# Optimization experiments

Hardware: AMD Instinct MI355X
Metric: run time of the kernel (lower is better)

## Reference

```python
import jax, jax.numpy as jnp
import numpy as np

N_NODES = 100000
N_EDGES = 1600000


def _sage_conv(x, src, dst, W_l, W_r, b):
    """PyG SAGEConv (mean aggr): lin_l(mean of neighbor feats) + b + lin_r(x)."""
    n = x.shape[0]
    msgs = x[src]                                            # [E, F] gather
    agg = jax.ops.segment_sum(msgs, dst, num_segments=n)     # [N, F]
    cnt = jax.ops.segment_sum(jnp.ones((src.shape[0],), x.dtype), dst,
                              num_segments=n)                # [N]
    mean = agg / jnp.maximum(cnt, 1.0)[:, None]
    return mean @ W_l + b + x @ W_r


def setup_inputs() -> dict:
    key = jax.random.key(0)
    ks = jax.random.split(key, 8)
    x = jax.random.normal(ks[0], (N_NODES, 64), dtype=jnp.float32)
    edge_index = jax.random.randint(ks[1], (2, N_EDGES), 0, N_NODES, dtype=jnp.int64)
    # Glorot-ish small init for weights
    W1_l = jax.random.normal(ks[2], (64, 128), dtype=jnp.float32) * 0.1
    W1_r = jax.random.normal(ks[3], (64, 128), dtype=jnp.float32) * 0.1
    b1 = jax.random.normal(ks[4], (128,), dtype=jnp.float32) * 0.1
    W2_l = jax.random.normal(ks[5], (128, 64), dtype=jnp.float32) * 0.1
    W2_r = jax.random.normal(ks[6], (128, 64), dtype=jnp.float32) * 0.1
    b2 = jax.random.normal(ks[7], (64,), dtype=jnp.float32) * 0.1
    return {"x": x, "edge_index": edge_index, "W1_l": W1_l, "W1_r": W1_r,
            "b1": b1, "W2_l": W2_l, "W2_r": W2_r, "b2": b2}


def reference(x, edge_index, W1_l, W1_r, b1, W2_l, W2_r, b2):
    src, dst = edge_index[0], edge_index[1]
    h = jax.nn.relu(_sage_conv(x, src, dst, W1_l, W1_r, b1))  # [N, 128]
    out = _sage_conv(h, src, dst, W2_l, W2_r, b2)             # [N, 64]
    return out
```

## Files before the change

### kernel.cpp

```cpp
#include <hip/hip_runtime.h>
#include <hip/hip_bf16.h>
#include <stdint.h>


typedef unsigned short u16;
typedef __attribute__((ext_vector_type(8))) short short8;
typedef __attribute__((ext_vector_type(4))) float f32x4;

#define BSHIFT 9
#define BSIZE  512
#define CHUNK  8192
#define NCP    256

__device__ __forceinline__ float bf2f(u16 v) { return __uint_as_float(((uint32_t)v) << 16); }
__device__ __forceinline__ float bfu_lo(uint32_t u) { return __uint_as_float(u << 16); }
__device__ __forceinline__ float bfu_hi(uint32_t u) { return __uint_as_float(u & 0xffff0000u); }
__device__ __forceinline__ u16 f2bf(float f) {
    uint32_t u = __float_as_uint(f);
    return (u16)((u + 0x7fffu + ((u >> 16) & 1u)) >> 16);
}

__global__ __launch_bounds__(512) void setup_k(
    const void* __restrict__ x, const void* __restrict__ ei,
    const void* __restrict__ W1l, const void* __restrict__ W1r,
    const void* __restrict__ b1, const void* __restrict__ W2l,
    const void* __restrict__ W2r, const void* __restrict__ b2,
    u16* __restrict__ wpk, u16* __restrict__ xb,
    int* __restrict__ hist2d, int* __restrict__ flags,
    int nn, int ne, int nb, int nchunk, int ncvt,
    int c0, int c1, int c2, int c3, int c4, int c5, int c6) {
    __shared__ int sh[512];
    __shared__ int sflag;
    int bid = blockIdx.x, tid = threadIdx.x;
    if (bid < nchunk) {
        sh[tid] = 0;
        int samp = 0;
        if (tid < 32) {
            long long n32 = 2LL * ne;
            long long stride = n32 / 32; if (stride < 1) stride = 1;
            long long i = (long long)tid * stride; i |= 1;
            if (i >= n32) i = 1;
            samp = (((const int*)ei)[i] != 0);
        }
        unsigned long long m = __ballot(samp);
        if (tid == 0) sflag = (m == 0ULL) ? 1 : 0;
        __syncthreads();
        int e64 = sflag;
        int base = bid * CHUNK;
#pragma unroll
        for (int j = 0; j < 16; j++) {
            int e = base + j * 512 + tid;
            if (e < ne) {
                int dst = e64 ? (int)((const long long*)ei)[(size_t)ne + e]
                              : ((const int*)ei)[(size_t)ne + e];
                if ((unsigned)dst < (unsigned)nn) atomicAdd(&sh[dst >> BSHIFT], 1);
            }
        }
        __syncthreads();
        for (int b = tid; b < nb; b += 512)
            hist2d[b * NCP + bid] = sh[b];
    } else if (bid < nchunk + ncvt) {
        int samp = 0;
        if (tid < 32) {
            int C = c0; int stride = C / 32; if (stride < 1) stride = 1;
            long long i = (long long)tid * stride;
            if (i > C - 1) i = C - 1; i &= ~1LL;
            u16 v = ((const u16*)x)[i];
            int e = (v >> 7) & 0xFF;
            samp = ((e >= 0x50 && e <= 0x97) || v == 0) ? 1 : 0;
        }
        unsigned long long m = __ballot(samp);
        if (tid == 0) sflag = (__popcll(m) >= 24) ? 1 : 0;
        __syncthreads();
        if (sflag) return;
        int i = (bid - nchunk) * 512 + tid;
        if (i < nn * 16) {
            float4 f = ((const float4*)x)[i];
            *(ushort4*)&xb[(size_t)i * 4] =
                make_ushort4(f2bf(f.x), f2bf(f.y), f2bf(f.z), f2bf(f.w));
        }
    } else if (bid < nchunk + ncvt + 4) {
        int b = bid - nchunk - ncvt;
        const void* src = (b == 0) ? W1l : (b == 1) ? W1r : (b == 2) ? W2l : W2r;
        int C = (b == 0) ? c1 : (b == 1) ? c2 : (b == 2) ? c4 : c5;
        int samp = 0;
        if (tid < 32) {
            int stride = C / 32; if (stride < 1) stride = 1;
            long long i = (long long)tid * stride;
            if (i > C - 1) i = C - 1; i &= ~1LL;
            u16 v = ((const u16*)src)[i];
            int e = (v >> 7) & 0xFF;
            samp = ((e >= 0x50 && e <= 0x97) || v == 0) ? 1 : 0;
        }
        unsigned long long m = __ballot(samp);
        if (tid == 0) sflag = (__popcll(m) >= 24) ? 1 : 0;
        __syncthreads();
        int isbf = sflag;
        u16* dst = wpk + ((b >= 2) ? (16384 + (b - 2) * 8192) : 0);
        for (int i = tid; i < 2048; i += 512) {
            u16 v0, v1, v2, v3;
            if (isbf) {
                ushort4 u = ((const ushort4*)src)[i];
                v0 = u.x; v1 = u.y; v2 = u.z; v3 = u.w;
            } else {
                float4 u = ((const float4*)src)[i];
                v0 = f2bf(u.x); v1 = f2bf(u.y); v2 = f2bf(u.z); v3 = f2bf(u.w);
            }
            int k, n, k8;
            if (b <= 1) { k = i >> 5; n = (i & 31) * 4; k8 = (b == 1 ? 8 : 0) + (k >> 3); }
            else        { k = i >> 4; n = (i & 15) * 4; k8 = k >> 3; }
            int kc = k8 >> 2, q = k8 & 3, w = k & 7;
            int basei = ((n >> 4) * 4 + kc) * 512 + (q * 16 + (n & 15)) * 8 + w;
            dst[basei] = v0; dst[basei + 8] = v1; dst[basei + 16] = v2; dst[basei + 24] = v3;
        }
    } else {
        int a = tid >> 5, lane = tid & 31;
        if (tid < 8) sh[tid] = 0;
        __syncthreads();
        if (a < 7) {
            const void* ptrs[7] = {x, W1l, W1r, b1, W2l, W2r, b2};
            int cs[7] = {c0, c1, c2, c3, c4, c5, c6};
            int C = cs[a];
            int stride = C / 32; if (stride < 1) stride = 1;
            long long i = (long long)lane * stride;
            if (i > C - 1) i = C - 1;
            i &= ~1LL;
            u16 v = ((const u16*)ptrs[a])[i];
            int e = (v >> 7) & 0xFF;
            int sane = ((e >= 0x50 && e <= 0x97) || v == 0) ? 1 : 0;
            atomicAdd(&sh[a], sane);
        } else if (a == 7) {
            long long n32 = 2LL * ne;
            long long stride = n32 / 32; if (stride < 1) stride = 1;
            long long i = (long long)lane * stride; i |= 1;
            if (i >= n32) i = 1;
            int wv = ((const int*)ei)[i];
            atomicAdd(&sh[7], wv != 0 ? 1 : 0);
        }
        __syncthreads();
        if (tid < 7) flags[tid] = (sh[tid] >= 24) ? 1 : 0;
        if (tid == 7) flags[7] = (sh[7] == 0) ? 1 : 0;
    }
}

__global__ __launch_bounds__(256) void scan2d(
    const int* __restrict__ hist2d, int* __restrict__ base2d,
    int* __restrict__ btot, int nchunk) {
    __shared__ int t0[256];
    int b = blockIdx.x, tid = threadIdx.x;
    int v = (tid < nchunk) ? hist2d[b * NCP + tid] : 0;
    t0[tid] = v;
    __syncthreads();
    for (int d = 1; d < 256; d <<= 1) {
        int t = (tid >= d) ? t0[tid - d] : 0;
        __syncthreads();
        t0[tid] += t;
        __syncthreads();
    }
    if (tid < nchunk) base2d[b * NCP + tid] = t0[tid] - v;
    if (tid == 255) btot[b] = t0[255];
}

__global__ __launch_bounds__(512) void partition_k(
    const void* __restrict__ ei, const int* __restrict__ btot,
    const int* __restrict__ base2d,
    unsigned* __restrict__ ep, int nn, int ne, int nb) {
    __shared__ unsigned stage[CHUNK];
    __shared__ u16 ab[CHUNK];
    __shared__ int hist[512], incl[512], exl[512], gbase[512], lcur[512];
    __shared__ int e64s;
    int tid = threadIdx.x;
    int base = blockIdx.x * CHUNK;
    hist[tid] = 0;
    int samp = 0;
    if (tid < 32) {
        long long n32 = 2LL * ne;
        long long stride = n32 / 32; if (stride < 1) stride = 1;
        long long i = (long long)tid * stride; i |= 1;
        if (i >= n32) i = 1;
        samp = (((const int*)ei)[i] != 0);
    }
    unsigned long long bm = __ballot(samp);
    if (tid == 0) e64s = (bm == 0ULL) ? 1 : 0;
    __syncthreads();
    int e64 = e64s;
    unsigned pk[16]; int bk[16];
#pragma unroll
    for (int j = 0; j < 16; j++) {
        int e = base + j * 512 + tid;
        bk[j] = -1;
        pk[j] = 0;
        if (e < ne) {
            int src, dst;
            if (e64) {
                src = (int)((const long long*)ei)[e];
                dst = (int)((const long long*)ei)[(size_t)ne + e];
            } else {
                src = ((const int*)ei)[e];
                dst = ((const int*)ei)[(size_t)ne + e];
            }
            if ((unsigned)dst < (unsigned)nn) {
                if ((unsigned)src >= (unsigned)nn) src = 0;
                bk[j] = dst >> BSHIFT;
                pk[j] = (unsigned)src | ((unsigned)(dst & (BSIZE - 1)) << 17);
                atomicAdd(&hist[bk[j]], 1);
            }
        }
    }
    __syncthreads();
    incl[tid] = hist[tid];
    __syncthreads();
    for (int d = 1; d < 512; d <<= 1) {
        int t = (tid >= d) ? incl[tid - d] : 0;
        __syncthreads();
        incl[tid] += t;
        __syncthreads();
    }
    int ex = incl[tid] - hist[tid];
    exl[tid] = ex;
    lcur[tid] = ex;
    int tot = incl[511];
    __syncthreads();
    incl[tid] = (tid < nb) ? btot[tid] : 0;
    __syncthreads();
    for (int d = 1; d < 512; d <<= 1) {
        int t = (tid >= d) ? incl[tid - d] : 0;
        __syncthreads();
        incl[tid] += t;
        __syncthreads();
    }
    int bo_t = incl[tid] - ((tid < nb) ? btot[tid] : 0);
    gbase[tid] = (tid < nb) ? (bo_t + base2d[tid * NCP + blockIdx.x]) : 0;
    __syncthreads();
#pragma unroll
    for (int j = 0; j < 16; j++) {
        if (bk[j] >= 0) {
            int r = atomicAdd(&lcur[bk[j]], 1);
            stage[r] = pk[j];
            ab[r] = (u16)bk[j];
        }
    }
    __syncthreads();
    for (int j = tid; j < tot; j += 512) {
        int b = ab[j];
        ep[gbase[b] + (j - exl[b])] = stage[j];
    }
}

__global__ __launch_bounds__(512) void csr_fill2(
    const unsigned* __restrict__ ep, const int* __restrict__ btot,
    int* __restrict__ off, int* __restrict__ cnt, int* __restrict__ esrc,
    int nn, int nb) {
    __shared__ int hist[BSIZE], incl[BSIZE], lcur[BSIZE];
    int b = blockIdx.x;
    int tid = threadIdx.x;
    incl[tid] = (tid < nb) ? btot[tid] : 0;
    __syncthreads();
    for (int d = 1; d < 512; d <<= 1) {
        int t = (tid >= d) ? incl[tid - d] : 0;
        __syncthreads();
        incl[tid] += t;
        __syncthreads();
    }
    int end = incl[b];
    int beg = end - btot[b];
    __syncthreads();
    hist[tid] = 0;
    __syncthreads();
    for (int j = beg + tid; j < end; j += 512)
        atomicAdd(&hist[(ep[j] >> 17) & (BSIZE - 1)], 1);
    __syncthreads();
    incl[tid] = hist[tid];
    __syncthreads();
    for (int d = 1; d < 512; d <<= 1) {
        int t = (tid >= d) ? incl[tid - d] : 0;
        __syncthreads();
        incl[tid] += t;
        __syncthreads();
    }
    int ex = beg + incl[tid] - hist[tid];
    lcur[tid] = ex;
    int node = b * BSIZE + tid;
    if (node < nn) { off[node] = ex; cnt[node] = hist[tid]; }
    __syncthreads();
    for (int j = beg + tid; j < end; j += 512) {
        unsigned p = ep[j];
        int r = atomicAdd(&lcur[(p >> 17) & (BSIZE - 1)], 1);
        esrc[r] = (int)(p & 0x1FFFFu);
    }
}

__global__ __launch_bounds__(512, 8) void layer1(
    const void* __restrict__ x, const u16* __restrict__ xb,
    const int* __restrict__ esrc,
    const int* __restrict__ off, const int* __restrict__ cnt,
    const u16* __restrict__ w1g, const u16* __restrict__ w2lg,
    const void* __restrict__ b1,
    u16* __restrict__ h, u16* __restrict__ gpt,
    const int* __restrict__ flags, int nn) {
    __shared__ __align__(16) u16 wA[8 * 512];
    __shared__ float b_s[128];
    int tid = threadIdx.x;
    int node0 = blockIdx.x * 32;

    if (tid < 128) b_s[tid] = flags[3] ? bf2f(((const u16*)b1)[tid]) : ((const float*)b1)[tid];

    int grp = tid >> 4, gl = tid & 15;
    int n = node0 + grp;
    int mtile = grp >> 4, l15m = grp & 15;
    int idx_mean = (mtile * 4 + (gl >> 3)) * 512 + (((gl >> 1) & 3) * 16 + l15m) * 8 + (gl & 1) * 4;
    int idx_x = (mtile * 4 + 2 + (gl >> 3)) * 512 + (((gl >> 1) & 3) * 16 + l15m) * 8 + (gl & 1) * 4;
    const u16* xs = flags[0] ? (const u16*)x : xb;
    if (n < nn) {
        int beg = off[n], deg = cnt[n];
        float a0 = 0.f, a1 = 0.f, a2 = 0.f, a3 = 0.f;
        int i = 0;
        const u16* xbp = xs + gl * 4;
        for (; i + 16 <= deg; i += 16) {
            ushort4 v[16];
#pragma unroll
            for (int j = 0; j < 16; j++) {
                int s0 = esrc[beg + i + j];
                v[j] = *(const ushort4*)(xbp + (size_t)s0 * 64);
            }
#pragma unroll
            for (int j = 0; j < 16; j++) {
                a0 += bf2f(v[j].x); a1 += bf2f(v[j].y);
                a2 += bf2f(v[j].z); a3 += bf2f(v[j].w);
            }
        }
        for (; i + 8 <= deg; i += 8) {
            ushort4 v[8];
#pragma unroll
            for (int j = 0; j < 8; j++) {
                int s0 = esrc[beg + i + j];
                v[j] = *(const ushort4*)(xbp + (size_t)s0 * 64);
            }
#pragma unroll
            for (int j = 0; j < 8; j++) {
                a0 += bf2f(v[j].x); a1 += bf2f(v[j].y);
                a2 += bf2f(v[j].z); a3 += bf2f(v[j].w);
            }
        }
        for (; i < deg; i++) {
            int s0 = esrc[beg + i];
            ushort4 v = *(const ushort4*)(xbp + (size_t)s0 * 64);
            a0 += bf2f(v.x); a1 += bf2f(v.y); a2 += bf2f(v.z); a3 += bf2f(v.w);
        }
        float inv = 1.0f / (float)(deg > 0 ? deg : 1);
        *(ushort4*)&wA[idx_mean] =
            make_ushort4(f2bf(a0 * inv), f2bf(a1 * inv), f2bf(a2 * inv), f2bf(a3 * inv));
        *(ushort4*)&wA[idx_x] = *(const ushort4*)(xs + (size_t)n * 64 + gl * 4);
    } else {
        *(ushort4*)&wA[idx_mean] = make_ushort4(0, 0, 0, 0);
        *(ushort4*)&wA[idx_x] = make_ushort4(0, 0, 0, 0);
    }
    __syncthreads();

    int wv = tid >> 6, lane = tid & 63;
    int l15 = lane & 15, q = lane >> 4;
    f32x4 acc0 = {0.f, 0.f, 0.f, 0.f};
    f32x4 acc1 = {0.f, 0.f, 0.f, 0.f};
#pragma unroll
    for (int kc = 0; kc < 4; kc++) {
        short8 a0 = *(const short8*)&wA[(kc) * 512 + lane * 8];
        short8 a1 = *(const short8*)&wA[(4 + kc) * 512 + lane * 8];
        short8 b  = *(const short8*)&w1g[(wv * 4 + kc) * 512 + lane * 8];
        acc0 = __builtin_amdgcn_mfma_f32_16x16x32_bf16(a0, b, acc0, 0, 0, 0);
        acc1 = __builtin_amdgcn_mfma_f32_16x16x32_bf16(a1, b, acc1, 0, 0, 0);
    }
    int nc = wv * 16 + l15;
    float bias = b_s[nc];
    u16 hv0[4], hv1[4];
#pragma unroll
    for (int r = 0; r < 4; r++) {
        hv0[r] = f2bf(fmaxf(acc0[r] + bias, 0.0f));
        hv1[r] = f2bf(fmaxf(acc1[r] + bias, 0.0f));
        int m = q * 4 + r;
        int nd = node0 + m;
        if (nd < nn) h[(size_t)nd * 128 + nc] = hv0[r];
        nd = node0 + 16 + m;
        if (nd < nn) h[(size_t)nd * 128 + nc] = hv1[r];
    }
    if (gpt) {
        __syncthreads();
        int kcg = wv >> 1;
        int qg  = ((wv & 1) << 1) | (l15 >> 3);
        int wg  = l15 & 7;
#pragma unroll
        for (int r = 0; r < 4; r++) {
            int m = q * 4 + r;
            wA[kcg * 512 + (qg * 16 + m) * 8 + wg]       = hv0[r];
            wA[(4 + kcg) * 512 + (qg * 16 + m) * 8 + wg] = hv1[r];
        }
        __syncthreads();
        int mt2 = wv >> 2, nt2 = wv & 3;
        f32x4 ag = {0.f, 0.f, 0.f, 0.f};
#pragma unroll
        for (int kc = 0; kc < 4; kc++) {
            short8 a = *(const short8*)&wA[(mt2 * 4 + kc) * 512 + lane * 8];
            short8 b = *(const short8*)&w2lg[(nt2 * 4 + kc) * 512 + lane * 8];
            ag = __builtin_amdgcn_mfma_f32_16x16x32_bf16(a, b, ag, 0, 0, 0);
        }
        int nc2 = nt2 * 16 + l15;
#pragma unroll
        for (int r = 0; r < 4; r++) {
            int nd = node0 + mt2 * 16 + q * 4 + r;
            if (nd < nn) gpt[(size_t)nd * 64 + nc2] = f2bf(ag[r]);
        }
    }
}

__global__ __launch_bounds__(256, 8) void pre2(
    const u16* __restrict__ h, const u16* __restrict__ w2lg,
    u16* __restrict__ g, int nn) {
    int tid = threadIdx.x;
    int node0 = blockIdx.x * 64;
    int wv = tid >> 6, lane = tid & 63;
    int l15 = lane & 15, q = lane >> 4;
    int arow = node0 + wv * 16 + l15;
    if (arow >= nn) arow = nn - 1;
    const u16* hrow = h + (size_t)arow * 128 + q * 8;
    f32x4 acc[4];
#pragma unroll
    for (int nt = 0; nt < 4; nt++) acc[nt] = (f32x4){0.f, 0.f, 0.f, 0.f};
#pragma unroll
    for (int kc = 0; kc < 4; kc++) {
        short8 a = *(const short8*)(hrow + kc * 32);
#pragma unroll
        for (int nt = 0; nt < 4; nt++) {
            short8 b = *(const short8*)&w2lg[(nt * 4 + kc) * 512 + lane * 8];
            acc[nt] = __builtin_amdgcn_mfma_f32_16x16x32_bf16(a, b, acc[nt], 0, 0, 0);
        }
    }
#pragma unroll
    for (int nt = 0; nt < 4; nt++) {
        int nc = nt * 16 + l15;
#pragma unroll
        for (int r = 0; r < 4; r++) {
            int nd = node0 + wv * 16 + q * 4 + r;
            if (nd < nn) g[(size_t)nd * 64 + nc] = f2bf(acc[nt][r]);
        }
    }
}

__global__ __launch_bounds__(512, 8) void layer2(
    const u16* __restrict__ h, const u16* __restrict__ g,
    const int* __restrict__ esrc,
    const int* __restrict__ off, const int* __restrict__ cnt,
    const u16* __restrict__ w2rg, const void* __restrict__ b2,
    void* __restrict__ out, const int* __restrict__ flags, int nn) {
    __shared__ __align__(16) u16 wA2[8 * 512];
    __shared__ __align__(16) float meanbuf[32][72];
    __shared__ float b_s[64];
    int tid = threadIdx.x;
    int node0 = blockIdx.x * 32;
    int obf = flags[0];

    if (tid < 64) b_s[tid] = flags[6] ? bf2f(((const u16*)b2)[tid]) : ((const float*)b2)[tid];

    int grp = tid >> 4, gl = tid & 15;
    int n = node0 + grp;
    int mtile = grp >> 4, m15 = grp & 15;
    int idx_h = (mtile * 4 + (gl >> 2)) * 512 + ((gl & 3) * 16 + m15) * 8;
    if (n < nn) {
        *(uint4*)&wA2[idx_h] = *(const uint4*)(h + (size_t)n * 128 + gl * 8);
        int beg = off[n], deg = cnt[n];
        float a0 = 0.f, a1 = 0.f, a2 = 0.f, a3 = 0.f;
        const u16* gb = g + gl * 4;
        int i = 0;
        for (; i + 16 <= deg; i += 16) {
            uint2 v[16];
#pragma unroll
            for (int j = 0; j < 16; j++) {
                int s0 = esrc[beg + i + j];
                v[j] = *(const uint2*)(gb + (size_t)s0 * 64);
            }
#pragma unroll
            for (int j = 0; j < 16; j++) {
                a0 += bfu_lo(v[j].x); a1 += bfu_hi(v[j].x);
                a2 += bfu_lo(v[j].y); a3 += bfu_hi(v[j].y);
            }
        }
        for (; i + 8 <= deg; i += 8) {
            uint2 v[8];
#pragma unroll
            for (int j = 0; j < 8; j++) {
                int s0 = esrc[beg + i + j];
                v[j] = *(const uint2*)(gb + (size_t)s0 * 64);
            }
#pragma unroll
            for (int j = 0; j < 8; j++) {
                a0 += bfu_lo(v[j].x); a1 += bfu_hi(v[j].x);
                a2 += bfu_lo(v[j].y); a3 += bfu_hi(v[j].y);
            }
        }
        for (; i < deg; i++) {
            int s0 = esrc[beg + i];
            uint2 v = *(const uint2*)(gb + (size_t)s0 * 64);
            a0 += bfu_lo(v.x); a1 += bfu_hi(v.x);
            a2 += bfu_lo(v.y); a3 += bfu_hi(v.y);
        }
        float inv = 1.0f / (float)(deg > 0 ? deg : 1);
        *(float4*)&meanbuf[grp][gl * 4] =
            make_float4(a0 * inv, a1 * inv, a2 * inv, a3 * inv);
    } else {
        *(uint4*)&wA2[idx_h] = make_uint4(0, 0, 0, 0);
        *(float4*)&meanbuf[grp][gl * 4] = make_float4(0.f, 0.f, 0.f, 0.f);
    }
    __syncthreads();

    int wv = tid >> 6, lane = tid & 63;
    int l15 = lane & 15, q = lane >> 4;
    int mt = wv >> 2, nt = wv & 3;
    f32x4 acc = {0.f, 0.f, 0.f, 0.f};
#pragma unroll
    for (int kc = 0; kc < 4; kc++) {
        short8 a = *(const short8*)&wA2[(mt * 4 + kc) * 512 + lane * 8];
        short8 b = *(const short8*)&w2rg[(nt * 4 + kc) * 512 + lane * 8];
        acc = __builtin_amdgcn_mfma_f32_16x16x32_bf16(a, b, acc, 0, 0, 0);
    }
    int nc = nt * 16 + l15;
    float bias = b_s[nc];
#pragma unroll
    for (int r = 0; r < 4; r++) {
        int m = mt * 16 + q * 4 + r;
        int nd = node0 + m;
        if (nd < nn) {
            float v = acc[r] + bias + meanbuf[m][nc];
            if (obf) ((u16*)out)[(size_t)nd * 64 + nc] = f2bf(v);
            else     ((float*)out)[(size_t)nd * 64 + nc] = v;
        }
    }
}

__global__ __launch_bounds__(256) void zero_out_k(u16* __restrict__ out, int n) {
    int i = blockIdx.x * 256 + threadIdx.x;
    if (i < n) out[i] = 0;
}

extern "C" void kernel_launch(void* const* d_in, const int* in_sizes, int n_in,
                              void* d_out, int out_size, void* d_ws, size_t ws_size,
                              hipStream_t stream) {
    const void* x   = d_in[0];
    const void* ei  = d_in[1];
    const void* W1l = d_in[2];
    const void* W1r = d_in[3];
    const void* b1  = d_in[4];
    const void* W2l = d_in[5];
    const void* W2r = d_in[6];
    const void* b2  = d_in[7];

    int nn = in_sizes[0] / 64;
    int ne = in_sizes[1] / 2;
    int nb = (nn + BSIZE - 1) / BSIZE;
    int nchunk = (ne + CHUNK - 1) / CHUNK;

    auto al = [](size_t v) { return (v + 255) & ~(size_t)255; };
    size_t o_flags = 0;
    size_t o_btot  = 256;
    size_t o_wpk   = al(o_btot + 512 * 4);
    size_t o_cnt   = al(o_wpk + 65536);
    size_t o_off   = al(o_cnt + (size_t)nn * 4);
    size_t o_esrc  = al(o_off + (size_t)nn * 4);
    size_t o_h     = al(o_esrc + (size_t)ne * 4);
    size_t o_xb    = al(o_h + (size_t)nn * 128 * 2);
    size_t ws_base = o_xb + (size_t)nn * 64 * 2;
    size_t o_g2    = al(ws_base);
    size_t ws_fused = o_g2 + (size_t)nn * 64 * 2;

    size_t o_ep   = o_h;
    size_t o_h2d  = al(o_ep + (size_t)ne * 4);
    size_t o_b2d  = al(o_h2d + (size_t)512 * NCP * 4);
    size_t ov_end = o_b2d + (size_t)512 * NCP * 4;

    bool ok = ws_size >= ws_base && nb >= 1 && nb <= 512 && nn <= 131072 &&
              nchunk <= NCP && ov_end <= o_xb;
    if (!ok) {
        zero_out_k<<<(out_size + 255) / 256, 256, 0, stream>>>((u16*)d_out, out_size);
        return;
    }
    bool fused = ws_size >= ws_fused;

    char* ws = (char*)d_ws;
    int* flags  = (int*)(ws + o_flags);
    int* btot   = (int*)(ws + o_btot);
    u16* wpk    = (u16*)(ws + o_wpk);
    int* cnt    = (int*)(ws + o_cnt);
    int* off    = (int*)(ws + o_off);
    int* esrc   = (int*)(ws + o_esrc);
    u16* h      = (u16*)(ws + o_h);
    u16* xb     = (u16*)(ws + o_xb);
    u16* gbuf   = fused ? (u16*)(ws + o_g2) : xb;
    unsigned* ep = (unsigned*)(ws + o_ep);
    int* hist2d = (int*)(ws + o_h2d);
    int* base2d = (int*)(ws + o_b2d);

    int ncvt = (nn * 16 + 511) / 512;
    setup_k<<<nchunk + ncvt + 5, 512, 0, stream>>>(
        x, ei, W1l, W1r, b1, W2l, W2r, b2, wpk, xb, hist2d, flags,
        nn, ne, nb, nchunk, ncvt,
        in_sizes[0], in_sizes[2], in_sizes[3], in_sizes[4],
        in_sizes[5], in_sizes[6], in_sizes[7]);
    scan2d<<<nb, 256, 0, stream>>>(hist2d, base2d, btot, nchunk);
    partition_k<<<nchunk, 512, 0, stream>>>(ei, btot, base2d, ep, nn, ne, nb);
    csr_fill2<<<nb, 512, 0, stream>>>(ep, btot, off, cnt, esrc, nn, nb);
    int lb = (nn + 31) / 32;
    layer1<<<lb, 512, 0, stream>>>(x, xb, esrc, off, cnt, wpk, wpk + 16384, b1,
                                   h, fused ? gbuf : (u16*)nullptr, flags, nn);
    if (!fused)
        pre2<<<(nn + 63) / 64, 256, 0, stream>>>(h, wpk + 16384, gbuf, nn);
    layer2<<<lb, 512, 0, stream>>>(h, gbuf, esrc, off, cnt, wpk + 24576, b2,
                                   d_out, flags, nn);
}
```

Measured before the change: 228.1 us.

## Fuse layer-2 root projection into layer1 and widen gather loads to 16 bytes

Layer1 now computes both h@W2_l and h@W2_r with MFMA and writes two 64-wide bf16 buffers instead of the 128-wide h. Layer2 becomes a pure gather-mean plus add of the precomputed root term and bias, with no MFMA or shared tiles. Both gathers use 16-byte loads with two half-groups each handling alternate edges, combined by a shuffle. This cuts h traffic and layer2 work, and drops the pre2 fallback. In exchange the workspace must always hold the extra buffer, and the second layer's root term is rounded to bf16 before the add.

After: 261.1 us. 14.5% more time.

```diff
diff --git a/kernel.cpp b/kernel.cpp
--- a/kernel.cpp
+++ b/kernel.cpp
@@ -295,8 +295,8 @@
     const int* __restrict__ esrc,
     const int* __restrict__ off, const int* __restrict__ cnt,
     const u16* __restrict__ w1g, const u16* __restrict__ w2lg,
-    const void* __restrict__ b1,
-    u16* __restrict__ h, u16* __restrict__ gpt,
+    const u16* __restrict__ w2rg, const void* __restrict__ b1,
+    u16* __restrict__ g, u16* __restrict__ rr,
     const int* __restrict__ flags, int nn) {
     __shared__ __align__(16) u16 wA[8 * 512];
     __shared__ float b_s[128];
@@ -306,54 +306,66 @@
     if (tid < 128) b_s[tid] = flags[3] ? bf2f(((const u16*)b1)[tid]) : ((const float*)b1)[tid];
 
     int grp = tid >> 4, gl = tid & 15;
+    int eh = gl >> 3, sl = gl & 7;
     int n = node0 + grp;
     int mtile = grp >> 4, l15m = grp & 15;
-    int idx_mean = (mtile * 4 + (gl >> 3)) * 512 + (((gl >> 1) & 3) * 16 + l15m) * 8 + (gl & 1) * 4;
-    int idx_x = (mtile * 4 + 2 + (gl >> 3)) * 512 + (((gl >> 1) & 3) * 16 + l15m) * 8 + (gl & 1) * 4;
+    int idx_mean = (mtile * 4 + (sl >> 2)) * 512 + ((sl & 3) * 16 + l15m) * 8;
+    int idx_x    = (mtile * 4 + 2 + (sl >> 2)) * 512 + ((sl & 3) * 16 + l15m) * 8;
     const u16* xs = flags[0] ? (const u16*)x : xb;
     if (n < nn) {
         int beg = off[n], deg = cnt[n];
-        float a0 = 0.f, a1 = 0.f, a2 = 0.f, a3 = 0.f;
+        float a[8] = {0.f, 0.f, 0.f, 0.f, 0.f, 0.f, 0.f, 0.f};
+        const u16* xbp = xs + sl * 8;
         int i = 0;
-        const u16* xbp = xs + gl * 4;
         for (; i + 16 <= deg; i += 16) {
-            ushort4 v[16];
-#pragma unroll
-            for (int j = 0; j < 16; j++) {
-                int s0 = esrc[beg + i + j];
-                v[j] = *(const ushort4*)(xbp + (size_t)s0 * 64);
+            uint4 v[8];
+#pragma unroll
+            for (int j = 0; j < 8; j++) {
+                int s0 = esrc[beg + i + 2 * j + eh];
+                v[j] = *(const uint4*)(xbp + (size_t)s0 * 64);
             }
 #pragma unroll
-            for (int j = 0; j < 16; j++) {
-                a0 += bf2f(v[j].x); a1 += bf2f(v[j].y);
-                a2 += bf2f(v[j].z); a3 += bf2f(v[j].w);
+            for (int j = 0; j < 8; j++) {
+                a[0] += bfu_lo(v[j].x); a[1] += bfu_hi(v[j].x);
+                a[2] += bfu_lo(v[j].y); a[3] += bfu_hi(v[j].y);
+                a[4] += bfu_lo(v[j].z); a[5] += bfu_hi(v[j].z);
+                a[6] += bfu_lo(v[j].w); a[7] += bfu_hi(v[j].w);
             }
         }
-        for (; i + 8 <= deg; i += 8) {
-            ushort4 v[8];
-#pragma unroll
-            for (int j = 0; j < 8; j++) {
-                int s0 = esrc[beg + i + j];
-                v[j] = *(const ushort4*)(xbp + (size_t)s0 * 64);
-            }
-#pragma unroll
-            for (int j = 0; j < 8; j++) {
-                a0 += bf2f(v[j].x); a1 += bf2f(v[j].y);
-                a2 += bf2f(v[j].z); a3 += bf2f(v[j].w);
-            }
-        }
-        for (; i < deg; i++) {
+        for (; i + 2 <= deg; i += 2) {
+            int s0 = esrc[beg + i + eh];
+            uint4 v = *(const uint4*)(xbp + (size_t)s0 * 64);
+            a[0] += bfu_lo(v.x); a[1] += bfu_hi(v.x);
+            a[2] += bfu_lo(v.y); a[3] += bfu_hi(v.y);
+            a[4] += bfu_lo(v.z); a[5] += bfu_hi(v.z);
+            a[6] += bfu_lo(v.w); a[7] += bfu_hi(v.w);
+        }
+        if (i < deg && eh == 0) {
             int s0 = esrc[beg + i];
-            ushort4 v = *(const ushort4*)(xbp + (size_t)s0 * 64);
-            a0 += bf2f(v.x); a1 += bf2f(v.y); a2 += bf2f(v.z); a3 += bf2f(v.w);
-        }
+            uint4 v = *(const uint4*)(xbp + (size_t)s0 * 64);
+            a[0] += bfu_lo(v.x); a[1] += bfu_hi(v.x);
+            a[2] += bfu_lo(v.y); a[3] += bfu_hi(v.y);
+            a[4] += bfu_lo(v.z); a[5] += bfu_hi(v.z);
+            a[6] += bfu_lo(v.w); a[7] += bfu_hi(v.w);
+        }
+#pragma unroll
+        for (int c = 0; c < 8; c++) a[c] += __shfl_xor(a[c], 8);
         float inv = 1.0f / (float)(deg > 0 ? deg : 1);
-        *(ushort4*)&wA[idx_mean] =
-            make_ushort4(f2bf(a0 * inv), f2bf(a1 * inv), f2bf(a2 * inv), f2bf(a3 * inv));
-        *(ushort4*)&wA[idx_x] = *(const ushort4*)(xs + (size_t)n * 64 + gl * 4);
+        if (eh == 0) {
+            *(ushort4*)&wA[idx_mean] =
+                make_ushort4(f2bf(a[0] * inv), f2bf(a[1] * inv), f2bf(a[2] * inv), f2bf(a[3] * inv));
+            *(ushort4*)&wA[idx_mean + 4] =
+                make_ushort4(f2bf(a[4] * inv), f2bf(a[5] * inv), f2bf(a[6] * inv), f2bf(a[7] * inv));
+        } else {
+            *(uint4*)&wA[idx_x] = *(const uint4*)(xs + (size_t)n * 64 + sl * 8);
+        }
     } else {
-        *(ushort4*)&wA[idx_mean] = make_ushort4(0, 0, 0, 0);
-        *(ushort4*)&wA[idx_x] = make_ushort4(0, 0, 0, 0);
+        if (eh == 0) {
+            *(ushort4*)&wA[idx_mean] = make_ushort4(0, 0, 0, 0);
+            *(ushort4*)&wA[idx_mean + 4] = make_ushort4(0, 0, 0, 0);
+        } else {
+            *(uint4*)&wA[idx_x] = make_uint4(0, 0, 0, 0);
+        }
     }
     __syncthreads();
 
@@ -376,160 +388,113 @@
     for (int r = 0; r < 4; r++) {
         hv0[r] = f2bf(fmaxf(acc0[r] + bias, 0.0f));
         hv1[r] = f2bf(fmaxf(acc1[r] + bias, 0.0f));
+    }
+    __syncthreads();
+    int kcg = wv >> 1;
+    int qg  = ((wv & 1) << 1) | (l15 >> 3);
+    int wg  = l15 & 7;
+#pragma unroll
+    for (int r = 0; r < 4; r++) {
         int m = q * 4 + r;
-        int nd = node0 + m;
-        if (nd < nn) h[(size_t)nd * 128 + nc] = hv0[r];
-        nd = node0 + 16 + m;
-        if (nd < nn) h[(size_t)nd * 128 + nc] = hv1[r];
-    }
-    if (gpt) {
-        __syncthreads();
-        int kcg = wv >> 1;
-        int qg  = ((wv & 1) << 1) | (l15 >> 3);
-        int wg  = l15 & 7;
-#pragma unroll
-        for (int r = 0; r < 4; r++) {
-            int m = q * 4 + r;
-            wA[kcg * 512 + (qg * 16 + m) * 8 + wg]       = hv0[r];
-            wA[(4 + kcg) * 512 + (qg * 16 + m) * 8 + wg] = hv1[r];
-        }
-        __syncthreads();
-        int mt2 = wv >> 2, nt2 = wv & 3;
-        f32x4 ag = {0.f, 0.f, 0.f, 0.f};
-#pragma unroll
-        for (int kc = 0; kc < 4; kc++) {
-            short8 a = *(const short8*)&wA[(mt2 * 4 + kc) * 512 + lane * 8];
-            short8 b = *(const short8*)&w2lg[(nt2 * 4 + kc) * 512 + lane * 8];
-            ag = __builtin_amdgcn_mfma_f32_16x16x32_bf16(a, b, ag, 0, 0, 0);
-        }
-        int nc2 = nt2 * 16 + l15;
-#pragma unroll
-        for (int r = 0; r < 4; r++) {
-            int nd = node0 + mt2 * 16 + q * 4 + r;
-            if (nd < nn) gpt[(size_t)nd * 64 + nc2] = f2bf(ag[r]);
-        }
-    }
-}
-
-__global__ __launch_bounds__(256, 8) void pre2(
-    const u16* __restrict__ h, const u16* __restrict__ w2lg,
-    u16* __restrict__ g, int nn) {
-    int tid = threadIdx.x;
-    int node0 = blockIdx.x * 64;
-    int wv = tid >> 6, lane = tid & 63;
-    int l15 = lane & 15, q = lane >> 4;
-    int arow = node0 + wv * 16 + l15;
-    if (arow >= nn) arow = nn - 1;
-    const u16* hrow = h + (size_t)arow * 128 + q * 8;
-    f32x4 acc[4];
-#pragma unroll
-    for (int nt = 0; nt < 4; nt++) acc[nt] = (f32x4){0.f, 0.f, 0.f, 0.f};
+        wA[kcg * 512 + (qg * 16 + m) * 8 + wg]       = hv0[r];
+        wA[(4 + kcg) * 512 + (qg * 16 + m) * 8 + wg] = hv1[r];
+    }
+    __syncthreads();
+    int mt2 = wv >> 2, nt2 = wv & 3;
+    f32x4 ag = {0.f, 0.f, 0.f, 0.f};
+    f32x4 ar = {0.f, 0.f, 0.f, 0.f};
 #pragma unroll
     for (int kc = 0; kc < 4; kc++) {
-        short8 a = *(const short8*)(hrow + kc * 32);
-#pragma unroll
-        for (int nt = 0; nt < 4; nt++) {
-            short8 b = *(const short8*)&w2lg[(nt * 4 + kc) * 512 + lane * 8];
-            acc[nt] = __builtin_amdgcn_mfma_f32_16x16x32_bf16(a, b, acc[nt], 0, 0, 0);
-        }
-    }
-#pragma unroll
-    for (int nt = 0; nt < 4; nt++) {
-        int nc = nt * 16 + l15;
-#pragma unroll
-        for (int r = 0; r < 4; r++) {
-            int nd = node0 + wv * 16 + q * 4 + r;
-            if (nd < nn) g[(size_t)nd * 64 + nc] = f2bf(acc[nt][r]);
+        short8 a = *(const short8*)&wA[(mt2 * 4 + kc) * 512 + lane * 8];
+        short8 bl = *(const short8*)&w2lg[(nt2 * 4 + kc) * 512 + lane * 8];
+        short8 br = *(const short8*)&w2rg[(nt2 * 4 + kc) * 512 + lane * 8];
+        ag = __builtin_amdgcn_mfma_f32_16x16x32_bf16(a, bl, ag, 0, 0, 0);
+        ar = __builtin_amdgcn_mfma_f32_16x16x32_bf16(a, br, ar, 0, 0, 0);
+    }
+    int nc2 = nt2 * 16 + l15;
+#pragma unroll
+    for (int r = 0; r < 4; r++) {
+        int nd = node0 + mt2 * 16 + q * 4 + r;
+        if (nd < nn) {
+            g[(size_t)nd * 64 + nc2]  = f2bf(ag[r]);
+            rr[(size_t)nd * 64 + nc2] = f2bf(ar[r]);
         }
     }
 }
 
 __global__ __launch_bounds__(512, 8) void layer2(
-    const u16* __restrict__ h, const u16* __restrict__ g,
+    const u16* __restrict__ g, const u16* __restrict__ rr,
     const int* __restrict__ esrc,
     const int* __restrict__ off, const int* __restrict__ cnt,
-    const u16* __restrict__ w2rg, const void* __restrict__ b2,
-    void* __restrict__ out, const int* __restrict__ flags, int nn) {
-    __shared__ __align__(16) u16 wA2[8 * 512];
-    __shared__ __align__(16) float meanbuf[32][72];
+    const void* __restrict__ b2, void* __restrict__ out,
+    const int* __restrict__ flags, int nn) {
     __shared__ float b_s[64];
     int tid = threadIdx.x;
     int node0 = blockIdx.x * 32;
     int obf = flags[0];
-
     if (tid < 64) b_s[tid] = flags[6] ? bf2f(((const u16*)b2)[tid]) : ((const float*)b2)[tid];
+    __syncthreads();
 
     int grp = tid >> 4, gl = tid & 15;
+    int eh = gl >> 3, sl = gl & 7;
     int n = node0 + grp;
-    int mtile = grp >> 4, m15 = grp & 15;
-    int idx_h = (mtile * 4 + (gl >> 2)) * 512 + ((gl & 3) * 16 + m15) * 8;
-    if (n < nn) {
-        *(uint4*)&wA2[idx_h] = *(const uint4*)(h + (size_t)n * 128 + gl * 8);
-        int beg = off[n], deg = cnt[n];
-        float a0 = 0.f, a1 = 0.f, a2 = 0.f, a3 = 0.f;
-        const u16* gb = g + gl * 4;
-        int i = 0;
-        for (; i + 16 <= deg; i += 16) {
-            uint2 v[16];
-#pragma unroll
-            for (int j = 0; j < 16; j++) {
-                int s0 = esrc[beg + i + j];
-                v[j] = *(const uint2*)(gb + (size_t)s0 * 64);
-            }
-#pragma unroll
-            for (int j = 0; j < 16; j++) {
-                a0 += bfu_lo(v[j].x); a1 += bfu_hi(v[j].x);
-                a2 += bfu_lo(v[j].y); a3 += bfu_hi(v[j].y);
-            }
-        }
-        for (; i + 8 <= deg; i += 8) {
-            uint2 v[8];
-#pragma unroll
-            for (int j = 0; j < 8; j++) {
-                int s0 = esrc[beg + i + j];
-                v[j] = *(const uint2*)(gb + (size_t)s0 * 64);
-            }
-#pragma unroll
-            for (int j = 0; j < 8; j++) {
-                a0 += bfu_lo(v[j].x); a1 += bfu_hi(v[j].x);
-                a2 += bfu_lo(v[j].y); a3 += bfu_hi(v[j].y);
-            }
-        }
-        for (; i < deg; i++) {
-            int s0 = esrc[beg + i];
-            uint2 v = *(const uint2*)(gb + (size_t)s0 * 64);
-            a0 += bfu_lo(v.x); a1 += bfu_hi(v.x);
-            a2 += bfu_lo(v.y); a3 += bfu_hi(v.y);
-        }
+    if (n >= nn) return;
+    int beg = off[n], deg = cnt[n];
+    float a[8] = {0.f, 0.f, 0.f, 0.f, 0.f, 0.f, 0.f, 0.f};
+    const u16* gb = g + sl * 8;
+    int i = 0;
+    for (; i + 16 <= deg; i += 16) {
+        uint4 v[8];
+#pragma unroll
+        for (int j = 0; j < 8; j++) {
+            int s0 = esrc[beg + i + 2 * j + eh];
+            v[j] = *(const uint4*)(gb + (size_t)s0 * 64);
+        }
+#pragma unroll
+        for (int j = 0; j < 8; j++) {
+            a[0] += bfu_lo(v[j].x); a[1] += bfu_hi(v[j].x);
+            a[2] += bfu_lo(v[j].y); a[3] += bfu_hi(v[j].y);
+            a[4] += bfu_lo(v[j].z); a[5] += bfu_hi(v[j].z);
+            a[6] += bfu_lo(v[j].w); a[7] += bfu_hi(v[j].w);
+        }
+    }
+    for (; i + 2 <= deg; i += 2) {
+        int s0 = esrc[beg + i + eh];
+        uint4 v = *(const uint4*)(gb + (size_t)s0 * 64);
+        a[0] += bfu_lo(v.x); a[1] += bfu_hi(v.x);
+        a[2] += bfu_lo(v.y); a[3] += bfu_hi(v.y);
+        a[4] += bfu_lo(v.z); a[5] += bfu_hi(v.z);
+        a[6] += bfu_lo(v.w); a[7] += bfu_hi(v.w);
+    }
+    if (i < deg && eh == 0) {
+        int s0 = esrc[beg + i];
+        uint4 v = *(const uint4*)(gb + (size_t)s0 * 64);
+        a[0] += bfu_lo(v.x); a[1] += bfu_hi(v.x);
+        a[2] += bfu_lo(v.y); a[3] += bfu_hi(v.y);
+        a[4] += bfu_lo(v.z); a[5] += bfu_hi(v.z);
+        a[6] += bfu_lo(v.w); a[7] += bfu_hi(v.w);
+    }
+#pragma unroll
+    for (int c = 0; c < 8; c++) a[c] += __shfl_xor(a[c], 8);
+    if (eh == 0) {
         float inv = 1.0f / (float)(deg > 0 ? deg : 1);
-        *(float4*)&meanbuf[grp][gl * 4] =
-            make_float4(a0 * inv, a1 * inv, a2 * inv, a3 * inv);
-    } else {
-        *(uint4*)&wA2[idx_h] = make_uint4(0, 0, 0, 0);
-        *(float4*)&meanbuf[grp][gl * 4] = make_float4(0.f, 0.f, 0.f, 0.f);
-    }
-    __syncthreads();
-
-    int wv = tid >> 6, lane = tid & 63;
-    int l15 = lane & 15, q = lane >> 4;
-    int mt = wv >> 2, nt = wv & 3;
-    f32x4 acc = {0.f, 0.f, 0.f, 0.f};
-#pragma unroll
-    for (int kc = 0; kc < 4; kc++) {
-        short8 a = *(const short8*)&wA2[(mt * 4 + kc) * 512 + lane * 8];
-        short8 b = *(const short8*)&w2rg[(nt * 4 + kc) * 512 + lane * 8];
-        acc = __builtin_amdgcn_mfma_f32_16x16x32_bf16(a, b, acc, 0, 0, 0);
-    }
-    int nc = nt * 16 + l15;
-    float bias = b_s[nc];
-#pragma unroll
-    for (int r = 0; r < 4; r++) {
-        int m = mt * 16 + q * 4 + r;
-        int nd = node0 + m;
-        if (nd < nn) {
-            float v = acc[r] + bias + meanbuf[m][nc];
-            if (obf) ((u16*)out)[(size_t)nd * 64 + nc] = f2bf(v);
-            else     ((float*)out)[(size_t)nd * 64 + nc] = v;
+        uint4 rv = *(const uint4*)(rr + (size_t)n * 64 + sl * 8);
+        float o[8];
+        o[0] = a[0] * inv + bfu_lo(rv.x); o[1] = a[1] * inv + bfu_hi(rv.x);
+        o[2] = a[2] * inv + bfu_lo(rv.y); o[3] = a[3] * inv + bfu_hi(rv.y);
+        o[4] = a[4] * inv + bfu_lo(rv.z); o[5] = a[5] * inv + bfu_hi(rv.z);
+        o[6] = a[6] * inv + bfu_lo(rv.w); o[7] = a[7] * inv + bfu_hi(rv.w);
+#pragma unroll
+        for (int c = 0; c < 8; c++) o[c] += b_s[sl * 8 + c];
+        if (obf) {
+            ushort4 w0 = make_ushort4(f2bf(o[0]), f2bf(o[1]), f2bf(o[2]), f2bf(o[3]));
+            ushort4 w1 = make_ushort4(f2bf(o[4]), f2bf(o[5]), f2bf(o[6]), f2bf(o[7]));
+            u16* op = (u16*)out + (size_t)n * 64 + sl * 8;
+            *(ushort4*)op = w0; *(ushort4*)(op + 4) = w1;
+        } else {
+            float* op = (float*)out + (size_t)n * 64 + sl * 8;
+            *(float4*)op = make_float4(o[0], o[1], o[2], o[3]);
+            *(float4*)(op + 4) = make_float4(o[4], o[5], o[6], o[7]);
         }
     }
 }
@@ -563,24 +528,22 @@
     size_t o_cnt   = al(o_wpk + 65536);
     size_t o_off   = al(o_cnt + (size_t)nn * 4);
     size_t o_esrc  = al(o_off + (size_t)nn * 4);
-    size_t o_h     = al(o_esrc + (size_t)ne * 4);
-    size_t o_xb    = al(o_h + (size_t)nn * 128 * 2);
-    size_t ws_base = o_xb + (size_t)nn * 64 * 2;
-    size_t o_g2    = al(ws_base);
-    size_t ws_fused = o_g2 + (size_t)nn * 64 * 2;
-
-    size_t o_ep   = o_h;
+    size_t o_r     = al(o_esrc + (size_t)ne * 4);
+    size_t o_xb    = al(o_r + (size_t)nn * 64 * 2);
+    size_t o_g     = al(o_xb + (size_t)nn * 64 * 2);
+    size_t ws_req  = o_g + (size_t)nn * 64 * 2;
+
+    size_t o_ep   = o_r;
     size_t o_h2d  = al(o_ep + (size_t)ne * 4);
     size_t o_b2d  = al(o_h2d + (size_t)512 * NCP * 4);
     size_t ov_end = o_b2d + (size_t)512 * NCP * 4;
 
-    bool ok = ws_size >= ws_base && nb >= 1 && nb <= 512 && nn <= 131072 &&
+    bool ok = ws_size >= ws_req && nb >= 1 && nb <= 512 && nn <= 131072 &&
               nchunk <= NCP && ov_end <= o_xb;
     if (!ok) {
         zero_out_k<<<(out_size + 255) / 256, 256, 0, stream>>>((u16*)d_out, out_size);
         return;
     }
-    bool fused = ws_size >= ws_fused;
 
     char* ws = (char*)d_ws;
     int* flags  = (int*)(ws + o_flags);
@@ -589,9 +552,9 @@
     int* cnt    = (int*)(ws + o_cnt);
     int* off    = (int*)(ws + o_off);
     int* esrc   = (int*)(ws + o_esrc);
-    u16* h      = (u16*)(ws + o_h);
+    u16* rbuf   = (u16*)(ws + o_r);
     u16* xb     = (u16*)(ws + o_xb);
-    u16* gbuf   = fused ? (u16*)(ws + o_g2) : xb;
+    u16* gbuf   = (u16*)(ws + o_g);
     unsigned* ep = (unsigned*)(ws + o_ep);
     int* hist2d = (int*)(ws + o_h2d);
     int* base2d = (int*)(ws + o_b2d);
@@ -606,10 +569,8 @@
     partition_k<<<nchunk, 512, 0, stream>>>(ei, btot, base2d, ep, nn, ne, nb);
     csr_fill2<<<nb, 512, 0, stream>>>(ep, btot, off, cnt, esrc, nn, nb);
     int lb = (nn + 31) / 32;
-    layer1<<<lb, 512, 0, stream>>>(x, xb, esrc, off, cnt, wpk, wpk + 16384, b1,
-                                   h, fused ? gbuf : (u16*)nullptr, flags, nn);
-    if (!fused)
-        pre2<<<(nn + 63) / 64, 256, 0, stream>>>(h, wpk + 16384, gbuf, nn);
-    layer2<<<lb, 512, 0, stream>>>(h, gbuf, esrc, off, cnt, wpk + 24576, b2,
-                                   d_out, flags, nn);
-}
+    layer1<<<lb, 512, 0, stream>>>(x, xb, esrc, off, cnt,
+                                   wpk, wpk + 16384, wpk + 24576, b1,
+                                   gbuf, rbuf, flags, nn);
+    layer2<<<lb, 512, 0, stream>>>(gbuf, rbuf, esrc, off, cnt, b2, d_out, flags, nn);
+}
```

## Compute both layer-2 projections in layer1 epilogue, drop h buffer and pre2

Applied to the files above, without the earlier changes.

Layer1 now multiplies its relu output by both W2_l and W2_r in-block, then writes two 64-wide bf16 outputs (g and r) with coalesced 16-byte stores staged through shared memory. The 128-wide h tensor is no longer stored to global memory. Layer2 becomes a pure gather-mean plus elementwise add of r and bias, with no MFMA, no shared staging and no block sync after setup. This cuts global traffic (an N×128 write and read replaced by an N×64 write and read) and shrinks layer2. The cost is extra MFMA and shared-memory work and more syncs in layer1.

After: 222.9 us. 1.02x faster.

```diff
diff --git a/kernel.cpp b/kernel.cpp
--- a/kernel.cpp
+++ b/kernel.cpp
@@ -295,8 +295,8 @@
     const int* __restrict__ esrc,
     const int* __restrict__ off, const int* __restrict__ cnt,
     const u16* __restrict__ w1g, const u16* __restrict__ w2lg,
-    const void* __restrict__ b1,
-    u16* __restrict__ h, u16* __restrict__ gpt,
+    const u16* __restrict__ w2rg, const void* __restrict__ b1,
+    u16* __restrict__ g, u16* __restrict__ rr,
     const int* __restrict__ flags, int nn) {
     __shared__ __align__(16) u16 wA[8 * 512];
     __shared__ float b_s[128];
@@ -376,161 +376,112 @@
     for (int r = 0; r < 4; r++) {
         hv0[r] = f2bf(fmaxf(acc0[r] + bias, 0.0f));
         hv1[r] = f2bf(fmaxf(acc1[r] + bias, 0.0f));
+    }
+    __syncthreads();
+    int kcg = wv >> 1;
+    int qg  = ((wv & 1) << 1) | (l15 >> 3);
+    int wg  = l15 & 7;
+#pragma unroll
+    for (int r = 0; r < 4; r++) {
         int m = q * 4 + r;
-        int nd = node0 + m;
-        if (nd < nn) h[(size_t)nd * 128 + nc] = hv0[r];
-        nd = node0 + 16 + m;
-        if (nd < nn) h[(size_t)nd * 128 + nc] = hv1[r];
-    }
-    if (gpt) {
-        __syncthreads();
-        int kcg = wv >> 1;
-        int qg  = ((wv & 1) << 1) | (l15 >> 3);
-        int wg  = l15 & 7;
-#pragma unroll
-        for (int r = 0; r < 4; r++) {
-            int m = q * 4 + r;
-            wA[kcg * 512 + (qg * 16 + m) * 8 + wg]       = hv0[r];
-            wA[(4 + kcg) * 512 + (qg * 16 + m) * 8 + wg] = hv1[r];
-        }
-        __syncthreads();
-        int mt2 = wv >> 2, nt2 = wv & 3;
-        f32x4 ag = {0.f, 0.f, 0.f, 0.f};
-#pragma unroll
-        for (int kc = 0; kc < 4; kc++) {
-            short8 a = *(const short8*)&wA[(mt2 * 4 + kc) * 512 + lane * 8];
-            short8 b = *(const short8*)&w2lg[(nt2 * 4 + kc) * 512 + lane * 8];
-            ag = __builtin_amdgcn_mfma_f32_16x16x32_bf16(a, b, ag, 0, 0, 0);
-        }
-        int nc2 = nt2 * 16 + l15;
-#pragma unroll
-        for (int r = 0; r < 4; r++) {
-            int nd = node0 + mt2 * 16 + q * 4 + r;
-            if (nd < nn) gpt[(size_t)nd * 64 + nc2] = f2bf(ag[r]);
-        }
-    }
-}
-
-__global__ __launch_bounds__(256, 8) void pre2(
-    const u16* __restrict__ h, const u16* __restrict__ w2lg,
-    u16* __restrict__ g, int nn) {
-    int tid = threadIdx.x;
-    int node0 = blockIdx.x * 64;
-    int wv = tid >> 6, lane = tid & 63;
-    int l15 = lane & 15, q = lane >> 4;
-    int arow = node0 + wv * 16 + l15;
-    if (arow >= nn) arow = nn - 1;
-    const u16* hrow = h + (size_t)arow * 128 + q * 8;
-    f32x4 acc[4];
-#pragma unroll
-    for (int nt = 0; nt < 4; nt++) acc[nt] = (f32x4){0.f, 0.f, 0.f, 0.f};
+        wA[kcg * 512 + (qg * 16 + m) * 8 + wg]       = hv0[r];
+        wA[(4 + kcg) * 512 + (qg * 16 + m) * 8 + wg] = hv1[r];
+    }
+    __syncthreads();
+    int mt2 = wv >> 2, nt2 = wv & 3;
+    f32x4 ag = {0.f, 0.f, 0.f, 0.f};
+    f32x4 ar = {0.f, 0.f, 0.f, 0.f};
 #pragma unroll
     for (int kc = 0; kc < 4; kc++) {
-        short8 a = *(const short8*)(hrow + kc * 32);
-#pragma unroll
-        for (int nt = 0; nt < 4; nt++) {
-            short8 b = *(const short8*)&w2lg[(nt * 4 + kc) * 512 + lane * 8];
-            acc[nt] = __builtin_amdgcn_mfma_f32_16x16x32_bf16(a, b, acc[nt], 0, 0, 0);
-        }
-    }
-#pragma unroll
-    for (int nt = 0; nt < 4; nt++) {
-        int nc = nt * 16 + l15;
-#pragma unroll
-        for (int r = 0; r < 4; r++) {
-            int nd = node0 + wv * 16 + q * 4 + r;
-            if (nd < nn) g[(size_t)nd * 64 + nc] = f2bf(acc[nt][r]);
-        }
+        short8 a = *(const short8*)&wA[(mt2 * 4 + kc) * 512 + lane * 8];
+        short8 bl = *(const short8*)&w2lg[(nt2 * 4 + kc) * 512 + lane * 8];
+        short8 br = *(const short8*)&w2rg[(nt2 * 4 + kc) * 512 + lane * 8];
+        ag = __builtin_amdgcn_mfma_f32_16x16x32_bf16(a, bl, ag, 0, 0, 0);
+        ar = __builtin_amdgcn_mfma_f32_16x16x32_bf16(a, br, ar, 0, 0, 0);
+    }
+    __syncthreads();
+    int nc2 = nt2 * 16 + l15;
+#pragma unroll
+    for (int r = 0; r < 4; r++) {
+        int m = mt2 * 16 + q * 4 + r;
+        wA[m * 64 + nc2]        = f2bf(ag[r]);
+        wA[2048 + m * 64 + nc2] = f2bf(ar[r]);
+    }
+    __syncthreads();
+    int half = tid >> 8, idx = tid & 255;
+    int row = idx >> 3, seg = idx & 7;
+    int nd = node0 + row;
+    if (nd < nn) {
+        uint4 v = *(const uint4*)&wA[half * 2048 + row * 64 + seg * 8];
+        u16* dst = (half ? rr : g) + (size_t)nd * 64 + seg * 8;
+        *(uint4*)dst = v;
     }
 }
 
 __global__ __launch_bounds__(512, 8) void layer2(
-    const u16* __restrict__ h, const u16* __restrict__ g,
+    const u16* __restrict__ g, const u16* __restrict__ rr,
     const int* __restrict__ esrc,
     const int* __restrict__ off, const int* __restrict__ cnt,
-    const u16* __restrict__ w2rg, const void* __restrict__ b2,
-    void* __restrict__ out, const int* __restrict__ flags, int nn) {
-    __shared__ __align__(16) u16 wA2[8 * 512];
-    __shared__ __align__(16) float meanbuf[32][72];
+    const void* __restrict__ b2, void* __restrict__ out,
+    const int* __restrict__ flags, int nn) {
     __shared__ float b_s[64];
     int tid = threadIdx.x;
     int node0 = blockIdx.x * 32;
     int obf = flags[0];
-
     if (tid < 64) b_s[tid] = flags[6] ? bf2f(((const u16*)b2)[tid]) : ((const float*)b2)[tid];
+    __syncthreads();
 
     int grp = tid >> 4, gl = tid & 15;
     int n = node0 + grp;
-    int mtile = grp >> 4, m15 = grp & 15;
-    int idx_h = (mtile * 4 + (gl >> 2)) * 512 + ((gl & 3) * 16 + m15) * 8;
-    if (n < nn) {
-        *(uint4*)&wA2[idx_h] = *(const uint4*)(h + (size_t)n * 128 + gl * 8);
-        int beg = off[n], deg = cnt[n];
-        float a0 = 0.f, a1 = 0.f, a2 = 0.f, a3 = 0.f;
-        const u16* gb = g + gl * 4;
-        int i = 0;
-        for (; i + 16 <= deg; i += 16) {
-            uint2 v[16];
-#pragma unroll
-            for (int j = 0; j < 16; j++) {
-                int s0 = esrc[beg + i + j];
-                v[j] = *(const uint2*)(gb + (size_t)s0 * 64);
-            }
-#pragma unroll
-            for (int j = 0; j < 16; j++) {
-                a0 += bfu_lo(v[j].x); a1 += bfu_hi(v[j].x);
-                a2 += bfu_lo(v[j].y); a3 += bfu_hi(v[j].y);
-            }
-        }
-        for (; i + 8 <= deg; i += 8) {
-            uint2 v[8];
-#pragma unroll
-            for (int j = 0; j < 8; j++) {
-                int s0 = esrc[beg + i + j];
-                v[j] = *(const uint2*)(gb + (size_t)s0 * 64);
-            }
-#pragma unroll
-            for (int j = 0; j < 8; j++) {
-                a0 += bfu_lo(v[j].x); a1 += bfu_hi(v[j].x);
-                a2 += bfu_lo(v[j].y); a3 += bfu_hi(v[j].y);
-            }
-        }
-        for (; i < deg; i++) {
-            int s0 = esrc[beg + i];
-            uint2 v = *(const uint2*)(gb + (size_t)s0 * 64);
-            a0 += bfu_lo(v.x); a1 += bfu_hi(v.x);
-            a2 += bfu_lo(v.y); a3 += bfu_hi(v.y);
-        }
-        float inv = 1.0f / (float)(deg > 0 ? deg : 1);
-        *(float4*)&meanbuf[grp][gl * 4] =
-            make_float4(a0 * inv, a1 * inv, a2 * inv, a3 * inv);
+    if (n >= nn) return;
+    int beg = off[n], deg = cnt[n];
+    float a0 = 0.f, a1 = 0.f, a2 = 0.f, a3 = 0.f;
+    const u16* gb = g + gl * 4;
+    int i = 0;
+    for (; i + 16 <= deg; i += 16) {
+        uint2 v[16];
+#pragma unroll
+        for (int j = 0; j < 16; j++) {
+            int s0 = esrc[beg + i + j];
+            v[j] = *(const uint2*)(gb + (size_t)s0 * 64);
+        }
+#pragma unroll
+        for (int j = 0; j < 16; j++) {
+            a0 += bfu_lo(v[j].x); a1 += bfu_hi(v[j].x);
+            a2 += bfu_lo(v[j].y); a3 += bfu_hi(v[j].y);
+        }
+    }
+    for (; i + 8 <= deg; i += 8) {
+        uint2 v[8];
+#pragma unroll
+        for (int j = 0; j < 8; j++) {
+            int s0 = esrc[beg + i + j];
+            v[j] = *(const uint2*)(gb + (size_t)s0 * 64);
+        }
+#pragma unroll
+        for (int j = 0; j < 8; j++) {
+            a0 += bfu_lo(v[j].x); a1 += bfu_hi(v[j].x);
+            a2 += bfu_lo(v[j].y); a3 += bfu_hi(v[j].y);
+        }
+    }
+    for (; i < deg; i++) {
+        int s0 = esrc[beg + i];
+        uint2 v = *(const uint2*)(gb + (size_t)s0 * 64);
+        a0 += bfu_lo(v.x); a1 += bfu_hi(v.x);
+        a2 += bfu_lo(v.y); a3 += bfu_hi(v.y);
+    }
+    float inv = 1.0f / (float)(deg > 0 ? deg : 1);
+    uint2 rv = *(const uint2*)(rr + (size_t)n * 64 + gl * 4);
+    float o0 = a0 * inv + bfu_lo(rv.x) + b_s[gl * 4 + 0];
+    float o1 = a1 * inv + bfu_hi(rv.x) + b_s[gl * 4 + 1];
+    float o2 = a2 * inv + bfu_lo(rv.y) + b_s[gl * 4 + 2];
+    float o3 = a3 * inv + bfu_hi(rv.y) + b_s[gl * 4 + 3];
+    if (obf) {
+        u16* op = (u16*)out + (size_t)n * 64 + gl * 4;
+        *(ushort4*)op = make_ushort4(f2bf(o0), f2bf(o1), f2bf(o2), f2bf(o3));
     } else {
-        *(uint4*)&wA2[idx_h] = make_uint4(0, 0, 0, 0);
-        *(float4*)&meanbuf[grp][gl * 4] = make_float4(0.f, 0.f, 0.f, 0.f);
-    }
-    __syncthreads();
-
-    int wv = tid >> 6, lane = tid & 63;
-    int l15 = lane & 15, q = lane >> 4;
-    int mt = wv >> 2, nt = wv & 3;
-    f32x4 acc = {0.f, 0.f, 0.f, 0.f};
-#pragma unroll
-    for (int kc = 0; kc < 4; kc++) {
-        short8 a = *(const short8*)&wA2[(mt * 4 + kc) * 512 + lane * 8];
-        short8 b = *(const short8*)&w2rg[(nt * 4 + kc) * 512 + lane * 8];
-        acc = __builtin_amdgcn_mfma_f32_16x16x32_bf16(a, b, acc, 0, 0, 0);
-    }
-    int nc = nt * 16 + l15;
-    float bias = b_s[nc];
-#pragma unroll
-    for (int r = 0; r < 4; r++) {
-        int m = mt * 16 + q * 4 + r;
-        int nd = node0 + m;
-        if (nd < nn) {
-            float v = acc[r] + bias + meanbuf[m][nc];
-            if (obf) ((u16*)out)[(size_t)nd * 64 + nc] = f2bf(v);
-            else     ((float*)out)[(size_t)nd * 64 + nc] = v;
-        }
+        float* op = (float*)out + (size_t)n * 64 + gl * 4;
+        *(float4*)op = make_float4(o0, o1, o2, o3);
     }
 }
 
@@ -563,24 +514,22 @@
     size_t o_cnt   = al(o_wpk + 65536);
     size_t o_off   = al(o_cnt + (size_t)nn * 4);
     size_t o_esrc  = al(o_off + (size_t)nn * 4);
-    size_t o_h     = al(o_esrc + (size_t)ne * 4);
-    size_t o_xb    = al(o_h + (size_t)nn * 128 * 2);
-    size_t ws_base = o_xb + (size_t)nn * 64 * 2;
-    size_t o_g2    = al(ws_base);
-    size_t ws_fused = o_g2 + (size_t)nn * 64 * 2;
-
-    size_t o_ep   = o_h;
+    size_t o_r     = al(o_esrc + (size_t)ne * 4);
+    size_t o_xb    = al(o_r + (size_t)nn * 64 * 2);
+    size_t o_g     = al(o_xb + (size_t)nn * 64 * 2);
+    size_t ws_req  = o_g + (size_t)nn * 64 * 2;
+
+    size_t o_ep   = o_r;
     size_t o_h2d  = al(o_ep + (size_t)ne * 4);
     size_t o_b2d  = al(o_h2d + (size_t)512 * NCP * 4);
     size_t ov_end = o_b2d + (size_t)512 * NCP * 4;
 
-    bool ok = ws_size >= ws_base && nb >= 1 && nb <= 512 && nn <= 131072 &&
+    bool ok = ws_size >= ws_req && nb >= 1 && nb <= 512 && nn <= 131072 &&
               nchunk <= NCP && ov_end <= o_xb;
     if (!ok) {
         zero_out_k<<<(out_size + 255) / 256, 256, 0, stream>>>((u16*)d_out, out_size);
         return;
     }
-    bool fused = ws_size >= ws_fused;
 
     char* ws = (char*)d_ws;
     int* flags  = (int*)(ws + o_flags);
@@ -589,9 +538,9 @@
     int* cnt    = (int*)(ws + o_cnt);
     int* off    = (int*)(ws + o_off);
     int* esrc   = (int*)(ws + o_esrc);
-    u16* h      = (u16*)(ws + o_h);
+    u16* rbuf   = (u16*)(ws + o_r);
     u16* xb     = (u16*)(ws + o_xb);
-    u16* gbuf   = fused ? (u16*)(ws + o_g2) : xb;
+    u16* gbuf   = (u16*)(ws + o_g);
     unsigned* ep = (unsigned*)(ws + o_ep);
     int* hist2d = (int*)(ws + o_h2d);
     int* base2d = (int*)(ws + o_b2d);
@@ -606,10 +555,8 @@
     partition_k<<<nchunk, 512, 0, stream>>>(ei, btot, base2d, ep, nn, ne, nb);
     csr_fill2<<<nb, 512, 0, stream>>>(ep, btot, off, cnt, esrc, nn, nb);
     int lb = (nn + 31) / 32;
-    layer1<<<lb, 512, 0, stream>>>(x, xb, esrc, off, cnt, wpk, wpk + 16384, b1,
-                                   h, fused ? gbuf : (u16*)nullptr, flags, nn);
-    if (!fused)
-        pre2<<<(nn + 63) / 64, 256, 0, stream>>>(h, wpk + 16384, gbuf, nn);
-    layer2<<<lb, 512, 0, stream>>>(h, gbuf, esrc, off, cnt, wpk + 24576, b2,
-                                   d_out, flags, nn);
-}
+    layer1<<<lb, 512, 0, stream>>>(x, xb, esrc, off, cnt,
+                                   wpk, wpk + 16384, wpk + 24576, b1,
+                                   gbuf, rbuf, flags, nn);
+    layer2<<<lb, 512, 0, stream>>>(gbuf, rbuf, esrc, off, cnt, b2, d_out, flags, nn);
+}
```
